# Kernel optimization log

Measured on AMD Instinct MI355X. Metric: run time of the kernel, lower is better.

## Reference

```python
import jax, jax.numpy as jnp
import numpy as np

NUM_LONGTERM_MEM = 16  # config.num_longterm_mem


def setup_inputs() -> dict:
    key = jax.random.key(0)
    ks = jax.random.split(key, 9)
    B, T, C, H = 32, 2048, 768, 1536
    s = 0.02
    return {
        "x": jax.random.normal(ks[0], (B, T, C), jnp.float32),
        "Wq": jax.random.normal(ks[1], (C, C), jnp.float32) * s,
        "bq": jax.random.normal(ks[2], (C,), jnp.float32) * s,
        "W0": jax.random.normal(ks[3], (B, H, C), jnp.float32) * s,
        "b0": jax.random.normal(ks[4], (B, H), jnp.float32) * s,
        "W1": jax.random.normal(ks[5], (B, C, H), jnp.float32) * s,
        "b1": jax.random.normal(ks[6], (B, C), jnp.float32) * s,
        "Wo": jax.random.normal(ks[7], (C, C), jnp.float32) * s,
        "bo": jax.random.normal(ks[8], (C,), jnp.float32) * s,
    }


def reference(x, Wq, bq, W0, b0, W1, b1, Wo, bo):
    # x: [B, T, C]. Per-sample memory MLP weights W0 [B,H,C], W1 [B,C,H].
    B, T, C = x.shape
    L = NUM_LONGTERM_MEM
    # query projection (nn.Linear: x @ W^T + b)
    q = jnp.einsum("btc,dc->btd", x, Wq) + bq                       # [B,T,C]
    # per-sample 2-layer memory MLP with SiLU
    h = jax.nn.silu(jnp.einsum("btc,bhc->bth", q, W0) + b0[:, None, :])  # [B,T,H]
    mem = jnp.einsum("bth,bch->btc", h, W1) + b1[:, None, :]        # [B,T,C]
    # adaptive_avg_pool1d over T -> L (T divisible by L => uniform window mean)
    pooled = mem.reshape(B, L, T // L, C).mean(axis=2)              # [B,L,C]
    # output projection
    return jnp.einsum("blc,dc->bld", pooled, Wo) + bo               # [B,L,C]
```

## Files before the change

kernel.cpp:

```cpp
#include <hip/hip_runtime.h>
#include <stdint.h>

#define B_ 32
#define T_ 2048
#define C_ 768
#define H_ 1536
#define L_ 16

typedef unsigned short u16;
typedef __bf16 bf16x8 __attribute__((ext_vector_type(8)));
typedef float f32x4 __attribute__((ext_vector_type(4)));

__device__ __forceinline__ u16 f2bf(float f) {
    union { float f; uint32_t u; } v; v.f = f;
    uint32_t r = (v.u + 0x7fffu + ((v.u >> 16) & 1u)) >> 16;
    return (u16)r;
}

__device__ __forceinline__ float wave_sum(float v) {
    v += __shfl_xor(v, 1);  v += __shfl_xor(v, 2);  v += __shfl_xor(v, 4);
    v += __shfl_xor(v, 8);  v += __shfl_xor(v, 16); v += __shfl_xor(v, 32);
    return v;
}

__global__ void k_cvt(const float* __restrict__ in, u16* __restrict__ out, int n4) {
    int stride = gridDim.x * blockDim.x;
    for (int i = blockIdx.x * blockDim.x + threadIdx.x; i < n4; i += stride) {
        float4 v = reinterpret_cast<const float4*>(in)[i];
        ushort4 o;
        o.x = f2bf(v.x); o.y = f2bf(v.y); o.z = f2bf(v.z); o.w = f2bf(v.w);
        reinterpret_cast<ushort4*>(out)[i] = o;
    }
}

__device__ __forceinline__ void gload16(const u16* g, u16* l) {
    __builtin_amdgcn_global_load_lds((const __attribute__((address_space(1))) void*)g,
                                     (__attribute__((address_space(3))) void*)l, 16, 0, 0);
}

template <int EPI>
__global__ __launch_bounds__(512, 2) void k_gemm8(const u16* __restrict__ Aall,
                                                  const u16* __restrict__ Ball,
                                                  const float* __restrict__ biasall,
                                                  u16* __restrict__ qout,
                                                  float* __restrict__ ph) {
    __shared__ u16 sm[65536];
    const int t = threadIdx.x;
    const int w = t >> 6, lane = t & 63;
    const int wr = w >> 2, wc = w & 3;
    const int l15 = lane & 15, kq = lane >> 4, cx = lane & 7;

    const int gx = gridDim.x, gy = gridDim.y;
    const int nwg = gx * gy * gridDim.z;
    int flat = blockIdx.x + gx * (blockIdx.y + gy * blockIdx.z);
    if ((nwg & 7) == 0) flat = (flat & 7) * (nwg >> 3) + (flat >> 3);
    const int bx = flat % gx;
    const int tmp = flat / gx;
    const int by = tmp % gy;
    const int bz = tmp / gy;

    const int n0 = bx * 256;
    const int m0 = by * 256;
    const u16* A; const u16* Bm; const float* bias;
    if constexpr (EPI == 0) {
        A = Aall + (size_t)m0 * C_;
        Bm = Ball + (size_t)n0 * C_;
        bias = biasall + n0;
    } else {
        A = Aall + ((size_t)bz * T_ + m0) * C_;
        Bm = Ball + ((size_t)bz * H_ + n0) * C_;
        bias = biasall + (size_t)bz * H_ + n0;
    }

    const int rl = (w << 4) + (lane >> 3);
    const int cs = (((lane & 7) ^ ((lane >> 3) & 7)) << 3);
    const int ldst = (w << 10);

    auto stA = [&](int kt, int h) {
        const u16* g = A + (size_t)(h * 128 + rl) * C_ + kt * 64 + cs;
        u16* l = sm + (kt & 1) * 32768 + h * 8192 + ldst;
        gload16(g, l);
        gload16(g + 8 * C_, l + 512);
    };
    auto stB = [&](int kt, int h) {
        const u16* g = Bm + (size_t)(h * 128 + rl) * C_ + kt * 64 + cs;
        u16* l = sm + (kt & 1) * 32768 + 16384 + h * 8192 + ldst;
        gload16(g, l);
        gload16(g + 8 * C_, l + 512);
    };

    f32x4 acc[8][4];
#pragma unroll
    for (int m = 0; m < 8; ++m)
#pragma unroll
        for (int n = 0; n < 4; ++n) acc[m][n] = (f32x4){0.f, 0.f, 0.f, 0.f};

    bf16x8 a0[4][2], a1[4][2], bfr[2][2];

    const int koff0 = ((kq ^ cx) << 3);
    const int koff1 = (((4 + kq) ^ cx) << 3);
    const u16* vA0 = sm + wr * 8192 + l15 * 64 + koff0;
    const u16* vA1 = sm + wr * 8192 + l15 * 64 + koff1;
    const u16* vB0 = sm + 16384 + (wc >> 1) * 8192 + (wc & 1) * 4096 + l15 * 64 + koff0;
    const u16* vB1 = sm + 16384 + (wc >> 1) * 8192 + (wc & 1) * 4096 + l15 * 64 + koff1;

    auto rdAB0 = [&](int bt) {
        const u16* A0 = vA0 + bt * 32768;
        const u16* A1 = vA1 + bt * 32768;
        const u16* B0 = vB0 + bt * 32768;
        const u16* B1 = vB1 + bt * 32768;
        bfr[0][0] = *reinterpret_cast<const bf16x8*>(B0);
        bfr[1][0] = *reinterpret_cast<const bf16x8*>(B0 + 1024);
        a0[0][0] = *reinterpret_cast<const bf16x8*>(A0);
        a0[1][0] = *reinterpret_cast<const bf16x8*>(A0 + 1024);
        a0[2][0] = *reinterpret_cast<const bf16x8*>(A0 + 2048);
        a0[3][0] = *reinterpret_cast<const bf16x8*>(A0 + 3072);
        bfr[0][1] = *reinterpret_cast<const bf16x8*>(B1);
        bfr[1][1] = *reinterpret_cast<const bf16x8*>(B1 + 1024);
        a0[0][1] = *reinterpret_cast<const bf16x8*>(A1);
        a0[1][1] = *reinterpret_cast<const bf16x8*>(A1 + 1024);
        a0[2][1] = *reinterpret_cast<const bf16x8*>(A1 + 2048);
        a0[3][1] = *reinterpret_cast<const bf16x8*>(A1 + 3072);
    };
    auto rdA1 = [&](int bt) {
        const u16* A0 = vA0 + bt * 32768 + 4096;
        const u16* A1 = vA1 + bt * 32768 + 4096;
        a1[0][0] = *reinterpret_cast<const bf16x8*>(A0);
        a1[1][0] = *reinterpret_cast<const bf16x8*>(A0 + 1024);
        a1[2][0] = *reinterpret_cast<const bf16x8*>(A0 + 2048);
        a1[3][0] = *reinterpret_cast<const bf16x8*>(A0 + 3072);
        a1[0][1] = *reinterpret_cast<const bf16x8*>(A1);
        a1[1][1] = *reinterpret_cast<const bf16x8*>(A1 + 1024);
        a1[2][1] = *reinterpret_cast<const bf16x8*>(A1 + 2048);
        a1[3][1] = *reinterpret_cast<const bf16x8*>(A1 + 3072);
    };
    auto rdB1 = [&](int bt) {
        const u16* B0 = vB0 + bt * 32768 + 2048;
        const u16* B1 = vB1 + bt * 32768 + 2048;
        bfr[0][0] = *reinterpret_cast<const bf16x8*>(B0);
        bfr[1][0] = *reinterpret_cast<const bf16x8*>(B0 + 1024);
        bfr[0][1] = *reinterpret_cast<const bf16x8*>(B1);
        bfr[1][1] = *reinterpret_cast<const bf16x8*>(B1 + 1024);
    };
    auto mma16 = [&](bf16x8 (&a)[4][2], int mq, int qn) {
        __builtin_amdgcn_s_setprio(1);
#pragma unroll
        for (int ks = 0; ks < 2; ++ks)
#pragma unroll
            for (int mm = 0; mm < 4; ++mm)
#pragma unroll
                for (int nn = 0; nn < 2; ++nn)
                    acc[mq * 4 + mm][qn * 2 + nn] = __builtin_amdgcn_mfma_f32_16x16x32_bf16(
                        a[mm][ks], bfr[nn][ks], acc[mq * 4 + mm][qn * 2 + nn], 0, 0, 0);
        __builtin_amdgcn_s_setprio(0);
    };

    auto ktile = [&](int kt, int bt) {
        rdAB0(bt);
        rdA1(bt);
        if (kt + 1 < 12) { stB(kt + 1, 0); stB(kt + 1, 1); }
        mma16(a0, 0, 0);
        mma16(a1, 1, 0);
        __builtin_amdgcn_s_barrier();
        rdB1(bt);
        const bool st = (kt + 2 < 12);
        if (st) { stA(kt + 2, 0); stA(kt + 2, 1); }
        mma16(a0, 0, 1);
        mma16(a1, 1, 1);
        if (st) asm volatile("s_waitcnt vmcnt(4)" ::: "memory");
        else    asm volatile("s_waitcnt vmcnt(0)" ::: "memory");
        __builtin_amdgcn_s_barrier();
    };

    stA(0, 0); stA(0, 1); stB(0, 0); stB(0, 1);
    stA(1, 0); stA(1, 1);
    asm volatile("s_waitcnt vmcnt(4)" ::: "memory");
    __builtin_amdgcn_s_barrier();

#pragma unroll 1
    for (int ktb = 0; ktb < 12; ktb += 2) {
        ktile(ktb, 0);
        ktile(ktb + 1, 1);
    }

    if constexpr (EPI == 0) {
        const int colb = n0 + wc * 64 + l15;
        const int rowb = m0 + wr * 128 + (kq << 2);
        float bv[4];
#pragma unroll
        for (int n = 0; n < 4; ++n) bv[n] = bias[wc * 64 + n * 16 + l15];
#pragma unroll
        for (int m = 0; m < 8; ++m)
#pragma unroll
            for (int r = 0; r < 4; ++r) {
                size_t ro = (size_t)(rowb + m * 16 + r) * C_;
#pragma unroll
                for (int n = 0; n < 4; ++n)
                    qout[ro + colb + n * 16] = f2bf(acc[m][n][r] + bv[n]);
            }
    } else {
        const int lwin = by * 2 + wr;
#pragma unroll
        for (int n = 0; n < 4; ++n) {
            int cloc = wc * 64 + n * 16 + l15;
            float bv = bias[cloc];
            float s = 0.f;
#pragma unroll
            for (int m = 0; m < 8; ++m)
#pragma unroll
                for (int r = 0; r < 4; ++r) {
                    float v = acc[m][n][r] + bv;
                    s += v / (1.f + __expf(-v));
                }
            s += __shfl_xor(s, 16);
            s += __shfl_xor(s, 32);
            if (kq == 0)
                ph[((size_t)bz * L_ + lwin) * H_ + n0 + cloc] = s * (1.f / 128.f);
        }
    }
}

__device__ __forceinline__ void stage_bf16_gload(const u16* gtile, int ld, u16* Ts,
                                                 int w, int lane) {
    const int r_in = lane >> 3;
    const int c0   = (lane & 7) << 3;
#pragma unroll
    for (int j = 0; j < 4; ++j) {
        int row = ((w << 2) + j) * 8 + r_in;
        const u16* g = gtile + (size_t)row * ld + c0;
        u16* l = Ts + (((w << 2) + j) << 9);
        gload16(g, l);
    }
}

__device__ __forceinline__ void stage_f32_cvt(const float* gtile, int ld, u16* Ts, int t) {
#pragma unroll
    for (int i = 0; i < 8; ++i) {
        int slot = t + (i << 8);
        int row  = slot >> 4;
        int c4   = (slot & 15) << 2;
        float4 v = *reinterpret_cast<const float4*>(gtile + (size_t)row * ld + c4);
        ushort4 o;
        o.x = f2bf(v.x); o.y = f2bf(v.y); o.z = f2bf(v.z); o.w = f2bf(v.w);
        *reinterpret_cast<ushort4*>(&Ts[row * 64 + c4]) = o;
    }
}

__device__ __forceinline__ void mfma_tile(const u16* As, const u16* Bs,
                                          f32x4 (&acc)[4][4], int wr, int wc, int lane) {
#pragma unroll
    for (int ks = 0; ks < 2; ++ks) {
        const int ko = (ks << 5) + ((lane >> 4) << 3);
        bf16x8 a[4], b[4];
#pragma unroll
        for (int m = 0; m < 4; ++m)
            a[m] = *reinterpret_cast<const bf16x8*>(&As[(wr * 64 + m * 16 + (lane & 15)) * 64 + ko]);
#pragma unroll
        for (int n = 0; n < 4; ++n)
            b[n] = *reinterpret_cast<const bf16x8*>(&Bs[(wc * 64 + n * 16 + (lane & 15)) * 64 + ko]);
#pragma unroll
        for (int m = 0; m < 4; ++m)
#pragma unroll
            for (int n = 0; n < 4; ++n)
                acc[m][n] = __builtin_amdgcn_mfma_f32_16x16x32_bf16(a[m], b[n], acc[m][n], 0, 0, 0);
    }
}

__global__ __launch_bounds__(256, 2) void k_gemm1(const float* __restrict__ x,
                                                  const u16* __restrict__ Wqb,
                                                  const float* __restrict__ bq,
                                                  u16* __restrict__ qb) {
    __shared__ u16 As[128 * 64];
    __shared__ u16 Bs[128 * 64];
    const int t = threadIdx.x, w = t >> 6, lane = t & 63;
    const int wr = w >> 1, wc = w & 1;
    const int m0 = blockIdx.y * 128;
    const int n0 = blockIdx.x * 128;

    f32x4 acc[4][4];
#pragma unroll
    for (int m = 0; m < 4; ++m)
#pragma unroll
        for (int n = 0; n < 4; ++n) acc[m][n] = (f32x4){0.f, 0.f, 0.f, 0.f};

    for (int kt = 0; kt < C_ / 64; ++kt) {
        stage_f32_cvt(x + (size_t)m0 * C_ + kt * 64, C_, As, t);
        stage_bf16_gload(Wqb + (size_t)n0 * C_ + kt * 64, C_, Bs, w, lane);
        __syncthreads();
        mfma_tile(As, Bs, acc, wr, wc, lane);
        __syncthreads();
    }

    const int r0 = m0 + wr * 64 + ((lane >> 4) << 2);
    const int cb = n0 + wc * 64 + (lane & 15);
#pragma unroll
    for (int n = 0; n < 4; ++n) {
        int c = cb + n * 16;
        float bb = bq[c];
#pragma unroll
        for (int m = 0; m < 4; ++m)
#pragma unroll
            for (int r = 0; r < 4; ++r)
                qb[(size_t)(r0 + m * 16 + r) * C_ + c] = f2bf(acc[m][n][r] + bb);
    }
}

template <bool BPRE>
__global__ __launch_bounds__(256, 2) void k_gemm2(const u16* __restrict__ qb,
                                                  const u16* __restrict__ W0b,
                                                  const float* __restrict__ W0f,
                                                  const float* __restrict__ b0,
                                                  float* __restrict__ ph) {
    __shared__ u16 As[128 * 64];
    __shared__ u16 Bs[128 * 64];
    __shared__ float Ps[2][128];
    const int t = threadIdx.x, w = t >> 6, lane = t & 63;
    const int wr = w >> 1, wc = w & 1;
    const int b  = blockIdx.z;
    const int mt = blockIdx.y;
    const int n0 = blockIdx.x * 128;
    const u16* Abase = qb + ((size_t)b * T_ + mt * 128) * C_;

    f32x4 acc[4][4];
#pragma unroll
    for (int m = 0; m < 4; ++m)
#pragma unroll
        for (int n = 0; n < 4; ++n) acc[m][n] = (f32x4){0.f, 0.f, 0.f, 0.f};

    for (int kt = 0; kt < C_ / 64; ++kt) {
        stage_bf16_gload(Abase + kt * 64, C_, As, w, lane);
        if (BPRE)
            stage_bf16_gload(W0b + ((size_t)b * H_ + n0) * C_ + kt * 64, C_, Bs, w, lane);
        else
            stage_f32_cvt(W0f + ((size_t)b * H_ + n0) * C_ + kt * 64, C_, Bs, t);
        __syncthreads();
        mfma_tile(As, Bs, acc, wr, wc, lane);
        __syncthreads();
    }

    float s[4];
#pragma unroll
    for (int n = 0; n < 4; ++n) {
        int c = n0 + wc * 64 + n * 16 + (lane & 15);
        float bb = b0[b * H_ + c];
        float sum = 0.f;
#pragma unroll
        for (int m = 0; m < 4; ++m)
#pragma unroll
            for (int r = 0; r < 4; ++r) {
                float v = acc[m][n][r] + bb;
                sum += v / (1.f + __expf(-v));
            }
        sum += __shfl_xor(sum, 16);
        sum += __shfl_xor(sum, 32);
        s[n] = sum;
    }
    if (lane < 16) {
#pragma unroll
        for (int n = 0; n < 4; ++n) Ps[wr][wc * 64 + n * 16 + lane] = s[n];
    }
    __syncthreads();
    if (t < 128)
        ph[((size_t)b * L_ + mt) * H_ + n0 + t] = (Ps[0][t] + Ps[1][t]) * (1.f / 128.f);
}

__global__ __launch_bounds__(256) void k_3a(const float* __restrict__ ph,
                                            const float* __restrict__ W1,
                                            const float* __restrict__ b1,
                                            float* __restrict__ pooled) {
    const int t = threadIdx.x, w = t >> 6, lane = t & 63;
    const int b  = blockIdx.y;
    const int cb = blockIdx.x * 16 + w * 4;

    float acc[4][16];
#pragma unroll
    for (int g = 0; g < 4; ++g)
#pragma unroll
        for (int l = 0; l < 16; ++l) acc[g][l] = 0.f;

    for (int i = 0; i < H_ / 256; ++i) {
        int h0 = i * 256 + lane * 4;
        float4 wv[4];
#pragma unroll
        for (int g = 0; g < 4; ++g)
            wv[g] = *reinterpret_cast<const float4*>(W1 + ((size_t)b * C_ + cb + g) * H_ + h0);
#pragma unroll
        for (int l = 0; l < 16; ++l) {
            float4 pv = *reinterpret_cast<const float4*>(ph + ((size_t)b * L_ + l) * H_ + h0);
#pragma unroll
            for (int g = 0; g < 4; ++g)
                acc[g][l] += wv[g].x * pv.x + wv[g].y * pv.y + wv[g].z * pv.z + wv[g].w * pv.w;
        }
    }
#pragma unroll
    for (int g = 0; g < 4; ++g)
#pragma unroll
        for (int l = 0; l < 16; ++l) acc[g][l] = wave_sum(acc[g][l]);

    if (lane < 16) {
#pragma unroll
        for (int g = 0; g < 4; ++g)
            pooled[((size_t)b * L_ + lane) * C_ + cb + g] = acc[g][lane] + b1[b * C_ + cb + g];
    }
}

__global__ __launch_bounds__(256) void k_3b(const float* __restrict__ pooled,
                                            const float* __restrict__ Wo,
                                            const float* __restrict__ bo,
                                            float* __restrict__ out) {
    __shared__ __align__(16) float ps[4 * 768];
    const int t = threadIdx.x, w = t >> 6, lane = t & 63;
    const int rr0 = blockIdx.x * 4;

    for (int idx = t; idx < 4 * 768; idx += 256)
        ps[idx] = pooled[(size_t)rr0 * 768 + idx];
    __syncthreads();

    for (int d = w; d < 768; d += 4) {
        float a0 = 0.f, a1 = 0.f, a2 = 0.f, a3 = 0.f;
#pragma unroll
        for (int i = 0; i < 3; ++i) {
            int c = i * 256 + lane * 4;
            float4 wv = *reinterpret_cast<const float4*>(Wo + (size_t)d * 768 + c);
            float4 p0 = *reinterpret_cast<const float4*>(&ps[0 * 768 + c]);
            float4 p1 = *reinterpret_cast<const float4*>(&ps[1 * 768 + c]);
            float4 p2 = *reinterpret_cast<const float4*>(&ps[2 * 768 + c]);
            float4 p3 = *reinterpret_cast<const float4*>(&ps[3 * 768 + c]);
            a0 += wv.x * p0.x + wv.y * p0.y + wv.z * p0.z + wv.w * p0.w;
            a1 += wv.x * p1.x + wv.y * p1.y + wv.z * p1.z + wv.w * p1.w;
            a2 += wv.x * p2.x + wv.y * p2.y + wv.z * p2.z + wv.w * p2.w;
            a3 += wv.x * p3.x + wv.y * p3.y + wv.z * p3.z + wv.w * p3.w;
        }
        a0 = wave_sum(a0); a1 = wave_sum(a1); a2 = wave_sum(a2); a3 = wave_sum(a3);
        if (lane == 0) {
            float bb = bo[d];
            out[(size_t)(rr0 + 0) * 768 + d] = a0 + bb;
            out[(size_t)(rr0 + 1) * 768 + d] = a1 + bb;
            out[(size_t)(rr0 + 2) * 768 + d] = a2 + bb;
            out[(size_t)(rr0 + 3) * 768 + d] = a3 + bb;
        }
    }
}

extern "C" void kernel_launch(void* const* d_in, const int* in_sizes, int n_in,
                              void* d_out, int out_size, void* d_ws, size_t ws_size,
                              hipStream_t stream) {
    const float* x  = (const float*)d_in[0];
    const float* Wq = (const float*)d_in[1];
    const float* bq = (const float*)d_in[2];
    const float* W0 = (const float*)d_in[3];
    const float* b0 = (const float*)d_in[4];
    const float* W1 = (const float*)d_in[5];
    const float* b1 = (const float*)d_in[6];
    const float* Wo = (const float*)d_in[7];
    const float* bo = (const float*)d_in[8];
    float* out = (float*)d_out;

    char* p = (char*)d_ws;
    size_t off = 0;
    auto carve = [&](size_t bytes) -> char* {
        char* r = p + off;
        off += (bytes + 255) & ~(size_t)255;
        return r;
    };
    u16*   qb     = (u16*)carve((size_t)B_ * T_ * C_ * 2);
    u16*   Wqb    = (u16*)carve((size_t)C_ * C_ * 2);
    float* ph     = (float*)carve((size_t)B_ * L_ * H_ * 4);
    float* pooled = (float*)carve((size_t)B_ * L_ * C_ * 4);

    const size_t xb_bytes  = (size_t)B_ * T_ * C_ * 2;
    const size_t w0b_bytes = (size_t)B_ * H_ * C_ * 2;

    if (off + xb_bytes <= ws_size) {
        u16* xb  = (u16*)carve(xb_bytes);
        u16* W0b = xb;

        k_cvt<<<dim3(2048), 256, 0, stream>>>(x, xb, B_ * T_ * C_ / 4);
        k_cvt<<<dim3(64), 256, 0, stream>>>(Wq, Wqb, C_ * C_ / 4);
        k_gemm8<0><<<dim3(C_ / 256, (B_ * T_) / 256), 512, 0, stream>>>(xb, Wqb, bq, qb, nullptr);
        k_cvt<<<dim3(2048), 256, 0, stream>>>(W0, W0b, B_ * H_ * C_ / 4);
        k_gemm8<1><<<dim3(H_ / 256, T_ / 256, B_), 512, 0, stream>>>(qb, W0b, b0, nullptr, ph);
    } else {
        u16* W0b = nullptr;
        if (off + w0b_bytes <= ws_size) W0b = (u16*)carve(w0b_bytes);

        k_cvt<<<dim3(64), 256, 0, stream>>>(Wq, Wqb, C_ * C_ / 4);
        if (W0b)
            k_cvt<<<dim3(2048), 256, 0, stream>>>(W0, W0b, B_ * H_ * C_ / 4);
        k_gemm1<<<dim3(C_ / 128, (B_ * T_) / 128), 256, 0, stream>>>(x, Wqb, bq, qb);
        if (W0b)
            k_gemm2<true><<<dim3(H_ / 128, L_, B_), 256, 0, stream>>>(qb, W0b, nullptr, b0, ph);
        else
            k_gemm2<false><<<dim3(H_ / 128, L_, B_), 256, 0, stream>>>(qb, nullptr, W0, b0, ph);
    }

    k_3a<<<dim3(C_ / 16, B_), 256, 0, stream>>>(ph, W1, b1, pooled);
    k_3b<<<dim3(B_ * L_ / 4), 256, 0, stream>>>(pooled, Wo, bo, out);
}
```

Baseline: 624.9 us.

## Fuse fp32-to-bf16 conversion of x and W0 into GEMM tile loads

Drops the separate conversion kernels for x and W0. Each GEMM now loads the fp32 operand tiles into registers, converts them to bf16 and writes them into swizzled LDS, while the already-bf16 operand still goes through direct global-to-LDS loads. The goal is to skip writing a full bf16 copy to memory and reading it back, plus two kernel launches. In exchange, fp32 global reads double the bytes per tile, raise register pressure, and the pipeline prefetch depth drops from two k-tiles to one, with stricter vmcnt(0) waits at every barrier.

Result: slower. 747.7 us (+19.6%).

```diff
diff --git a/kernel.cpp b/kernel.cpp
--- a/kernel.cpp
+++ b/kernel.cpp
@@ -39,8 +39,8 @@
 }
 
 template <int EPI>
-__global__ __launch_bounds__(512, 2) void k_gemm8(const u16* __restrict__ Aall,
-                                                  const u16* __restrict__ Ball,
+__global__ __launch_bounds__(512, 2) void k_gemmF(const u16* __restrict__ Gsrc,
+                                                  const float* __restrict__ Fsrc,
                                                   const float* __restrict__ biasall,
                                                   u16* __restrict__ qout,
                                                   float* __restrict__ ph) {
@@ -61,32 +61,48 @@
 
     const int n0 = bx * 256;
     const int m0 = by * 256;
-    const u16* A; const u16* Bm; const float* bias;
+    const u16* Gbase; const float* Fbase; const float* bias;
+    int Goff, Foff;
     if constexpr (EPI == 0) {
-        A = Aall + (size_t)m0 * C_;
-        Bm = Ball + (size_t)n0 * C_;
-        bias = biasall + n0;
+        Fbase = Fsrc + (size_t)m0 * C_;            Foff = 0;
+        Gbase = Gsrc + (size_t)n0 * C_;            Goff = 16384;
+        bias  = biasall + n0;
     } else {
-        A = Aall + ((size_t)bz * T_ + m0) * C_;
-        Bm = Ball + ((size_t)bz * H_ + n0) * C_;
-        bias = biasall + (size_t)bz * H_ + n0;
+        Gbase = Gsrc + ((size_t)bz * T_ + m0) * C_; Goff = 0;
+        Fbase = Fsrc + ((size_t)bz * H_ + n0) * C_; Foff = 16384;
+        bias  = biasall + (size_t)bz * H_ + n0;
     }
 
     const int rl = (w << 4) + (lane >> 3);
     const int cs = (((lane & 7) ^ ((lane >> 3) & 7)) << 3);
     const int ldst = (w << 10);
-
-    auto stA = [&](int kt, int h) {
-        const u16* g = A + (size_t)(h * 128 + rl) * C_ + kt * 64 + cs;
-        u16* l = sm + (kt & 1) * 32768 + h * 8192 + ldst;
+    auto stG = [&](int kt, int h) {
+        const u16* g = Gbase + (size_t)(h * 128 + rl) * C_ + kt * 64 + cs;
+        u16* l = sm + (kt & 1) * 32768 + Goff + h * 8192 + ldst;
         gload16(g, l);
         gload16(g + 8 * C_, l + 512);
     };
-    auto stB = [&](int kt, int h) {
-        const u16* g = Bm + (size_t)(h * 128 + rl) * C_ + kt * 64 + cs;
-        u16* l = sm + (kt & 1) * 32768 + 16384 + h * 8192 + ldst;
-        gload16(g, l);
-        gload16(g + 8 * C_, l + 512);
+
+    const int fr = t >> 4;
+    const int fc = t & 15;
+    const int fswz = ((fc >> 1) ^ (fr & 7));
+    const int fsub = (fc & 1) * 4;
+    float4 fg0[4], fg1[4];
+    auto fissue = [&](int kt, int b, float4 (&fregs)[4]) {
+#pragma unroll
+        for (int p = 0; p < 4; ++p)
+            fregs[p] = *reinterpret_cast<const float4*>(
+                Fbase + (size_t)(b * 128 + p * 32 + fr) * C_ + kt * 64 + fc * 4);
+    };
+    auto fwrite = [&](int bdst, int b, float4 (&fregs)[4]) {
+        u16* base = sm + Foff + bdst * 32768 + b * 8192 + fr * 64 + fswz * 8 + fsub;
+#pragma unroll
+        for (int p = 0; p < 4; ++p) {
+            ushort4 o;
+            o.x = f2bf(fregs[p].x); o.y = f2bf(fregs[p].y);
+            o.z = f2bf(fregs[p].z); o.w = f2bf(fregs[p].w);
+            *reinterpret_cast<ushort4*>(base + p * 2048) = o;
+        }
     };
 
     f32x4 acc[8][4];
@@ -155,27 +171,43 @@
         __builtin_amdgcn_s_setprio(0);
     };
 
+    fissue(0, 0, fg0);
+    fissue(0, 1, fg1);
+    stG(0, 0); stG(0, 1);
+    asm volatile("s_waitcnt vmcnt(8)" ::: "memory");
+    fwrite(0, 0, fg0);
+    asm volatile("s_waitcnt vmcnt(4)" ::: "memory");
+    fwrite(0, 1, fg1);
+    asm volatile("s_waitcnt lgkmcnt(0)" ::: "memory");
+    asm volatile("s_waitcnt vmcnt(0)" ::: "memory");
+    __builtin_amdgcn_sched_barrier(0);
+    __builtin_amdgcn_s_barrier();
+
     auto ktile = [&](int kt, int bt) {
+        const bool nx = (kt + 1 < 12);
+        if (nx) fissue(kt + 1, 0, fg0);
         rdAB0(bt);
         rdA1(bt);
-        if (kt + 1 < 12) { stB(kt + 1, 0); stB(kt + 1, 1); }
         mma16(a0, 0, 0);
+        if (nx) {
+            fissue(kt + 1, 1, fg1);
+            stG(kt + 1, 0); stG(kt + 1, 1);
+        }
         mma16(a1, 1, 0);
+        asm volatile("s_waitcnt vmcnt(8)" ::: "memory");
+        if (nx) fwrite(bt ^ 1, 0, fg0);
+        __builtin_amdgcn_sched_barrier(0);
         __builtin_amdgcn_s_barrier();
         rdB1(bt);
-        const bool st = (kt + 2 < 12);
-        if (st) { stA(kt + 2, 0); stA(kt + 2, 1); }
         mma16(a0, 0, 1);
         mma16(a1, 1, 1);
-        if (st) asm volatile("s_waitcnt vmcnt(4)" ::: "memory");
-        else    asm volatile("s_waitcnt vmcnt(0)" ::: "memory");
+        asm volatile("s_waitcnt vmcnt(4)" ::: "memory");
+        if (nx) fwrite(bt ^ 1, 1, fg1);
+        asm volatile("s_waitcnt lgkmcnt(0)" ::: "memory");
+        asm volatile("s_waitcnt vmcnt(0)" ::: "memory");
+        __builtin_amdgcn_sched_barrier(0);
         __builtin_amdgcn_s_barrier();
     };
-
-    stA(0, 0); stA(0, 1); stB(0, 0); stB(0, 1);
-    stA(1, 0); stA(1, 1);
-    asm volatile("s_waitcnt vmcnt(4)" ::: "memory");
-    __builtin_amdgcn_s_barrier();
 
 #pragma unroll 1
     for (int ktb = 0; ktb < 12; ktb += 2) {
@@ -468,18 +500,12 @@
     float* ph     = (float*)carve((size_t)B_ * L_ * H_ * 4);
     float* pooled = (float*)carve((size_t)B_ * L_ * C_ * 4);
 
-    const size_t xb_bytes  = (size_t)B_ * T_ * C_ * 2;
     const size_t w0b_bytes = (size_t)B_ * H_ * C_ * 2;
 
-    if (off + xb_bytes <= ws_size) {
-        u16* xb  = (u16*)carve(xb_bytes);
-        u16* W0b = xb;
-
-        k_cvt<<<dim3(2048), 256, 0, stream>>>(x, xb, B_ * T_ * C_ / 4);
+    if (off <= ws_size) {
         k_cvt<<<dim3(64), 256, 0, stream>>>(Wq, Wqb, C_ * C_ / 4);
-        k_gemm8<0><<<dim3(C_ / 256, (B_ * T_) / 256), 512, 0, stream>>>(xb, Wqb, bq, qb, nullptr);
-        k_cvt<<<dim3(2048), 256, 0, stream>>>(W0, W0b, B_ * H_ * C_ / 4);
-        k_gemm8<1><<<dim3(H_ / 256, T_ / 256, B_), 512, 0, stream>>>(qb, W0b, b0, nullptr, ph);
+        k_gemmF<0><<<dim3(C_ / 256, (B_ * T_) / 256), 512, 0, stream>>>(Wqb, x, bq, qb, nullptr);
+        k_gemmF<1><<<dim3(H_ / 256, T_ / 256, B_), 512, 0, stream>>>(qb, W0, b0, nullptr, ph);
     } else {
         u16* W0b = nullptr;
         if (off + w0b_bytes <= ws_size) W0b = (u16*)carve(w0b_bytes);
```
